# Kernel tuning notes

Measured on AMD Instinct MI355X. Metric: run time of the kernel, lower is better.

Reference implementation:

```python
import jax, jax.numpy as jnp
import numpy as np

B, F, CIN, COUT, K, R = 128, 1024, 16, 16, 4, 2


def setup_inputs() -> dict:
    key = jax.random.key(0)
    k1, k2 = jax.random.split(key)
    ll = jax.random.normal(k1, (B, F, CIN, R), dtype=jnp.float32)
    logits = jax.random.normal(k2, (COUT, CIN, K, K, R), dtype=jnp.float32)
    return {"ll": ll, "logits": logits, "kernel_size": K}


def reference(ll, logits, kernel_size):
    # ll: (B, F, Cin, R); logits: (O, Cin, K, K, R)
    b, f, cin, r = ll.shape
    o = logits.shape[0]
    k = kernel_size
    h = w = int(round(f ** 0.5))
    hb, wb = h // k, w // k
    # normalize weights over input channels (sum_dim=1)
    log_w = jax.nn.log_softmax(logits, axis=1)          # (O, Cin, K, K, R)
    # im2col-like patch reshape: (B, Cin, hb, wb, K, K, R)
    x = jnp.transpose(ll, (0, 2, 1, 3)).reshape(b, cin, hb, k, wb, k, r)
    x = jnp.transpose(x, (0, 1, 2, 4, 3, 5, 6))
    # broadcast-add log weights per kernel position, reduce over Cin
    w_b = log_w[None, :, :, None, None, :, :, :]        # (1, O, Cin, 1, 1, K, K, R)
    out = jax.nn.logsumexp(x[:, None] + w_b, axis=2)    # (B, O, hb, wb, K, K, R)
    # reassemble spatial grid and flatten back to features
    out = jnp.transpose(out, (0, 1, 2, 4, 3, 5, 6)).reshape(b, o, h, w, r)
    out = out.reshape(b, o, f, r)
    return jnp.transpose(out, (0, 2, 1, 3))             # (B, F, O, R)
```

## Files before the change

kernel.cpp:

```cpp
#include <hip/hip_runtime.h>


#define WSTRIDE 520
#define ESTRIDE 36

__global__ __launch_bounds__(256, 4) void sumconv_fused(
    const float* __restrict__ ll, const float* __restrict__ logits,
    float* __restrict__ out) {
  __shared__ float sw[8 * WSTRIDE + 64 * ESTRIDE];
  float* __restrict__ swW = sw;
  float* __restrict__ swE = sw + 8 * WSTRIDE;

  const int tid = threadIdx.x;
  const int blk = blockIdx.x;
  const int f_base = (blk * 64) & 1023;
  const int kkbase = ((f_base >> 5) & 3) * 4;

  {
    const int r = tid & 1, kkloc = (tid >> 1) & 7, o = tid >> 4;
    const int kk = kkbase + kkloc;
    const float* __restrict__ lg = logits + o * 512 + kk * 2 + r;
    float v[16];
    float m = -1e30f;
#pragma unroll
    for (int ci = 0; ci < 16; ++ci) {
      v[ci] = lg[ci * 32];
      m = fmaxf(m, v[ci]);
    }
    float sum = 0.f;
#pragma unroll
    for (int ci = 0; ci < 16; ++ci) {
      v[ci] = __expf(v[ci] - m);
      sum += v[ci];
    }
    const float inv = 1.0f / sum;
#pragma unroll
    for (int ci = 0; ci < 16; ++ci)
      swW[kkloc * WSTRIDE + ci * 32 + o * 2 + r] = v[ci] * inv;
  }

  {
    const float4* __restrict__ src = (const float4*)(ll + (size_t)blk * 2048);
#pragma unroll
    for (int j = 0; j < 2; ++j) {
      const int p = tid + 256 * j;
      const float4 v = src[p];
      const int row = p >> 3, c4 = p & 7;
      *(float4*)(swE + row * ESTRIDE + c4 * 4) =
          make_float4(__expf(v.x), __expf(v.y), __expf(v.z), __expf(v.w));
    }
  }
  __syncthreads();

  const int row = tid >> 2, q = tid & 3;
  const int i = blk * 64 + row;
  const int f = i & 1023;
  const int kk = (((f >> 5) & 3) << 2) | (f & 3);
  const float* __restrict__ wb = swW + (kk & 7) * WSTRIDE + q * 4;
  const float* __restrict__ eb = swE + row * ESTRIDE;

  float Ef[32];
#pragma unroll
  for (int k = 0; k < 8; ++k)
    *(float4*)(Ef + 4 * k) = *(const float4*)(eb + 4 * k);

  float4* __restrict__ op = (float4*)(out + (size_t)i * 32);
#pragma unroll 1
  for (int oo = 0; oo < 2; ++oo) {
    float a00 = 0.f, a01 = 0.f, a10 = 0.f, a11 = 0.f;
#pragma unroll
    for (int ci = 0; ci < 16; ++ci) {
      const float4 w = *(const float4*)(wb + ci * 32 + oo * 16);
      a00 = fmaf(w.x, Ef[2 * ci + 0], a00);
      a01 = fmaf(w.y, Ef[2 * ci + 1], a01);
      a10 = fmaf(w.z, Ef[2 * ci + 0], a10);
      a11 = fmaf(w.w, Ef[2 * ci + 1], a11);
    }
    op[q + 4 * oo] = make_float4(__logf(a00), __logf(a01), __logf(a10), __logf(a11));
  }
}

extern "C" void kernel_launch(void* const* d_in, const int* in_sizes, int n_in,
                              void* d_out, int out_size, void* d_ws, size_t ws_size,
                              hipStream_t stream) {
  const float* ll     = (const float*)d_in[0];
  const float* logits = (const float*)d_in[1];
  float* out = (float*)d_out;
  sumconv_fused<<<2048, 256, 0, stream>>>(ll, logits, out);
}
```

Before: 15.13 us.

## Process four batches per block to amortize weight softmax across batches

Each block now covers 64 features for 4 batch entries instead of 64 features for one, so the per-block log-softmax over logits and the weight reads from shared memory are reused across four batches. The grid shrinks from 2048 to 512 blocks, shared memory for exponentiated inputs grows fourfold, and launch bounds drop to 2 blocks per CU. In exchange, register pressure rises (128 Ef values plus 16 accumulators) and fewer blocks are available to hide latency.

```diff
diff --git a/kernel.cpp b/kernel.cpp
--- a/kernel.cpp
+++ b/kernel.cpp
@@ -4,17 +4,18 @@
 #define WSTRIDE 520
 #define ESTRIDE 36
 
-__global__ __launch_bounds__(256, 4) void sumconv_fused(
+__global__ __launch_bounds__(256, 2) void sumconv_fused(
     const float* __restrict__ ll, const float* __restrict__ logits,
     float* __restrict__ out) {
-  __shared__ float sw[8 * WSTRIDE + 64 * ESTRIDE];
+  __shared__ float sw[8 * WSTRIDE + 256 * ESTRIDE];
   float* __restrict__ swW = sw;
   float* __restrict__ swE = sw + 8 * WSTRIDE;
 
   const int tid = threadIdx.x;
   const int blk = blockIdx.x;
-  const int f_base = (blk * 64) & 1023;
-  const int kkbase = ((f_base >> 5) & 3) * 4;
+  const int f0 = (blk & 15) * 64;
+  const int b0 = (blk >> 4) * 4;
+  const int kkbase = ((f0 >> 5) & 3) * 4;
 
   {
     const int r = tid & 1, kkloc = (tid >> 1) & 7, o = tid >> 4;
@@ -39,44 +40,58 @@
       swW[kkloc * WSTRIDE + ci * 32 + o * 2 + r] = v[ci] * inv;
   }
 
-  {
-    const float4* __restrict__ src = (const float4*)(ll + (size_t)blk * 2048);
 #pragma unroll
-    for (int j = 0; j < 2; ++j) {
-      const int p = tid + 256 * j;
+  for (int j = 0; j < 4; ++j) {
+    const float4* __restrict__ src =
+        (const float4*)(ll + ((size_t)(b0 + j) * 1024 + f0) * 32);
+#pragma unroll
+    for (int m2 = 0; m2 < 2; ++m2) {
+      const int p = tid + 256 * m2;
       const float4 v = src[p];
       const int row = p >> 3, c4 = p & 7;
-      *(float4*)(swE + row * ESTRIDE + c4 * 4) =
+      *(float4*)(swE + (j * 64 + row) * ESTRIDE + c4 * 4) =
           make_float4(__expf(v.x), __expf(v.y), __expf(v.z), __expf(v.w));
     }
   }
   __syncthreads();
 
   const int row = tid >> 2, q = tid & 3;
-  const int i = blk * 64 + row;
-  const int f = i & 1023;
+  const int f = f0 + row;
   const int kk = (((f >> 5) & 3) << 2) | (f & 3);
   const float* __restrict__ wb = swW + (kk & 7) * WSTRIDE + q * 4;
-  const float* __restrict__ eb = swE + row * ESTRIDE;
 
-  float Ef[32];
+  float Ef[4][32];
 #pragma unroll
-  for (int k = 0; k < 8; ++k)
-    *(float4*)(Ef + 4 * k) = *(const float4*)(eb + 4 * k);
+  for (int j = 0; j < 4; ++j) {
+    const float* __restrict__ eb = swE + (j * 64 + row) * ESTRIDE;
+#pragma unroll
+    for (int k = 0; k < 8; ++k)
+      *(float4*)(&Ef[j][4 * k]) = *(const float4*)(eb + 4 * k);
+  }
 
-  float4* __restrict__ op = (float4*)(out + (size_t)i * 32);
-#pragma unroll 1
+#pragma unroll
   for (int oo = 0; oo < 2; ++oo) {
-    float a00 = 0.f, a01 = 0.f, a10 = 0.f, a11 = 0.f;
+    float a[4][4];
+#pragma unroll
+    for (int j = 0; j < 4; ++j)
+      a[j][0] = a[j][1] = a[j][2] = a[j][3] = 0.f;
 #pragma unroll
     for (int ci = 0; ci < 16; ++ci) {
       const float4 w = *(const float4*)(wb + ci * 32 + oo * 16);
-      a00 = fmaf(w.x, Ef[2 * ci + 0], a00);
-      a01 = fmaf(w.y, Ef[2 * ci + 1], a01);
-      a10 = fmaf(w.z, Ef[2 * ci + 0], a10);
-      a11 = fmaf(w.w, Ef[2 * ci + 1], a11);
+#pragma unroll
+      for (int j = 0; j < 4; ++j) {
+        a[j][0] = fmaf(w.x, Ef[j][2 * ci + 0], a[j][0]);
+        a[j][1] = fmaf(w.y, Ef[j][2 * ci + 1], a[j][1]);
+        a[j][2] = fmaf(w.z, Ef[j][2 * ci + 0], a[j][2]);
+        a[j][3] = fmaf(w.w, Ef[j][2 * ci + 1], a[j][3]);
+      }
     }
-    op[q + 4 * oo] = make_float4(__logf(a00), __logf(a01), __logf(a10), __logf(a11));
+#pragma unroll
+    for (int j = 0; j < 4; ++j) {
+      const size_t i = (size_t)(b0 + j) * 1024 + f;
+      ((float4*)(out + i * 32))[q + 4 * oo] = make_float4(
+          __logf(a[j][0]), __logf(a[j][1]), __logf(a[j][2]), __logf(a[j][3]));
+    }
   }
 }
 
@@ -86,5 +101,5 @@
   const float* ll     = (const float*)d_in[0];
   const float* logits = (const float*)d_in[1];
   float* out = (float*)d_out;
-  sumconv_fused<<<2048, 256, 0, stream>>>(ll, logits, out);
+  sumconv_fused<<<512, 256, 0, stream>>>(ll, logits, out);
 }
```

New measurement: 14.07 us. -7.0%, faster.

## Process four batch slabs per block with register-cached weights and prefetched loads

Applied to the files above, without the earlier changes.

Each block now handles four batches of the same 64-feature tile, so the log-softmax weight setup is amortized over four slabs and the weights are held in registers. Input loads for later slabs are issued ahead of time to overlap with compute, using separate LDS slabs and raw barriers in place of __syncthreads. The grid shrinks from 2048 to 512 blocks and launch bounds drop to 2 blocks per SM. In exchange, register pressure and LDS use go up and there is less parallelism to hide latency.

```diff
diff --git a/kernel.cpp b/kernel.cpp
--- a/kernel.cpp
+++ b/kernel.cpp
@@ -3,23 +3,34 @@
 
 #define WSTRIDE 520
 #define ESTRIDE 36
+#define ESLAB (64 * ESTRIDE)
 
-__global__ __launch_bounds__(256, 4) void sumconv_fused(
+#define EXP4(v) make_float4(__expf(v.x), __expf(v.y), __expf(v.z), __expf(v.w))
+
+__global__ __launch_bounds__(256, 2) void sumconv_fused(
     const float* __restrict__ ll, const float* __restrict__ logits,
     float* __restrict__ out) {
-  __shared__ float sw[8 * WSTRIDE + 64 * ESTRIDE];
+  __shared__ float sw[8 * WSTRIDE + 4 * ESLAB];
   float* __restrict__ swW = sw;
   float* __restrict__ swE = sw + 8 * WSTRIDE;
 
   const int tid = threadIdx.x;
   const int blk = blockIdx.x;
-  const int f_base = (blk * 64) & 1023;
-  const int kkbase = ((f_base >> 5) & 3) * 4;
+  const int f0 = (blk & 15) * 64;
+  const int b0 = (blk >> 4) * 4;
+  const int kkbase = ((f0 >> 5) & 3) * 4;
+
+  const float4* __restrict__ s0 = (const float4*)(ll + ((size_t)(b0 + 0) * 1024 + f0) * 32);
+  const float4* __restrict__ s1 = (const float4*)(ll + ((size_t)(b0 + 1) * 1024 + f0) * 32);
+  const float4* __restrict__ s2 = (const float4*)(ll + ((size_t)(b0 + 2) * 1024 + f0) * 32);
+  const float4* __restrict__ s3 = (const float4*)(ll + ((size_t)(b0 + 3) * 1024 + f0) * 32);
+  float4 L0a = s0[tid], L0b = s0[tid + 256];
+  float4 L1a = s1[tid], L1b = s1[tid + 256];
+  float4 L2a, L2b, L3a, L3b;
 
   {
     const int r = tid & 1, kkloc = (tid >> 1) & 7, o = tid >> 4;
-    const int kk = kkbase + kkloc;
-    const float* __restrict__ lg = logits + o * 512 + kk * 2 + r;
+    const float* __restrict__ lg = logits + o * 512 + (kkbase + kkloc) * 2 + r;
     float v[16];
     float m = -1e30f;
 #pragma unroll
@@ -38,46 +49,56 @@
     for (int ci = 0; ci < 16; ++ci)
       swW[kkloc * WSTRIDE + ci * 32 + o * 2 + r] = v[ci] * inv;
   }
-
-  {
-    const float4* __restrict__ src = (const float4*)(ll + (size_t)blk * 2048);
-#pragma unroll
-    for (int j = 0; j < 2; ++j) {
-      const int p = tid + 256 * j;
-      const float4 v = src[p];
-      const int row = p >> 3, c4 = p & 7;
-      *(float4*)(swE + row * ESTRIDE + c4 * 4) =
-          make_float4(__expf(v.x), __expf(v.y), __expf(v.z), __expf(v.w));
-    }
-  }
-  __syncthreads();
+  asm volatile("s_waitcnt lgkmcnt(0)" ::: "memory");
+  __builtin_amdgcn_s_barrier();
 
   const int row = tid >> 2, q = tid & 3;
-  const int i = blk * 64 + row;
-  const int f = i & 1023;
+  const int f = f0 + row;
   const int kk = (((f >> 5) & 3) << 2) | (f & 3);
   const float* __restrict__ wb = swW + (kk & 7) * WSTRIDE + q * 4;
-  const float* __restrict__ eb = swE + row * ESTRIDE;
+  float4 W0[16], W1[16];
+#pragma unroll
+  for (int ci = 0; ci < 16; ++ci) {
+    W0[ci] = *(const float4*)(wb + ci * 32);
+    W1[ci] = *(const float4*)(wb + ci * 32 + 16);
+  }
 
-  float Ef[32];
-#pragma unroll
-  for (int k = 0; k < 8; ++k)
-    *(float4*)(Ef + 4 * k) = *(const float4*)(eb + 4 * k);
+#define SLAB_BODY(J, A, B, ISSUE)                                             \
+  {                                                                           \
+    ISSUE               \
+    float* __restrict__ ew = swE + (J) * ESLAB;                               \
+    *(float4*)(ew + (tid >> 3) * ESTRIDE + (tid & 7) * 4) = EXP4(A);          \
+    *(float4*)(ew + ((tid >> 3) + 32) * ESTRIDE + (tid & 7) * 4) = EXP4(B);   \
+    asm volatile("s_waitcnt lgkmcnt(0)" ::: "memory");                        \
+    __builtin_amdgcn_s_barrier();                                             \
+    const float* __restrict__ ebr = swE + (J) * ESLAB + row * ESTRIDE;        \
+    float Ef[32];                                                             \
+    _Pragma("unroll")                                                         \
+    for (int k2 = 0; k2 < 8; ++k2)                                            \
+      *(float4*)(Ef + 4 * k2) = *(const float4*)(ebr + 4 * k2);               \
+    float4* __restrict__ op =                                                 \
+        (float4*)(out + ((size_t)(b0 + (J)) * 1024 + f) * 32);                \
+    _Pragma("unroll")                                                         \
+    for (int oo = 0; oo < 2; ++oo) {                                          \
+      float a0 = 0.f, a1 = 0.f, a2 = 0.f, a3 = 0.f;                           \
+      _Pragma("unroll")                                                       \
+      for (int ci = 0; ci < 16; ++ci) {                                       \
+        const float4 w = oo ? W1[ci] : W0[ci];                                \
+        a0 = fmaf(w.x, Ef[2 * ci + 0], a0);                                   \
+        a1 = fmaf(w.y, Ef[2 * ci + 1], a1);                                   \
+        a2 = fmaf(w.z, Ef[2 * ci + 0], a2);                                   \
+        a3 = fmaf(w.w, Ef[2 * ci + 1], a3);                                   \
+      }                                                                       \
+      op[q + 4 * oo] =                                                        \
+          make_float4(__logf(a0), __logf(a1), __logf(a2), __logf(a3));        \
+    }                                                                         \
+  }
 
-  float4* __restrict__ op = (float4*)(out + (size_t)i * 32);
-#pragma unroll 1
-  for (int oo = 0; oo < 2; ++oo) {
-    float a00 = 0.f, a01 = 0.f, a10 = 0.f, a11 = 0.f;
-#pragma unroll
-    for (int ci = 0; ci < 16; ++ci) {
-      const float4 w = *(const float4*)(wb + ci * 32 + oo * 16);
-      a00 = fmaf(w.x, Ef[2 * ci + 0], a00);
-      a01 = fmaf(w.y, Ef[2 * ci + 1], a01);
-      a10 = fmaf(w.z, Ef[2 * ci + 0], a10);
-      a11 = fmaf(w.w, Ef[2 * ci + 1], a11);
-    }
-    op[q + 4 * oo] = make_float4(__logf(a00), __logf(a01), __logf(a10), __logf(a11));
-  }
+  SLAB_BODY(0, L0a, L0b, L2a = s2[tid]; L2b = s2[tid + 256];)
+  SLAB_BODY(1, L1a, L1b, L3a = s3[tid]; L3b = s3[tid + 256];)
+  SLAB_BODY(2, L2a, L2b, ;)
+  SLAB_BODY(3, L3a, L3b, ;)
+#undef SLAB_BODY
 }
 
 extern "C" void kernel_launch(void* const* d_in, const int* in_sizes, int n_in,
@@ -86,5 +107,5 @@
   const float* ll     = (const float*)d_in[0];
   const float* logits = (const float*)d_in[1];
   float* out = (float*)d_out;
-  sumconv_fused<<<2048, 256, 0, stream>>>(ll, logits, out);
+  sumconv_fused<<<512, 256, 0, stream>>>(ll, logits, out);
 }
```

Result: faster. 14.16 us (-6.4%).

## Process two batches per block to amortize weight softmax and reuse weights

Applied to the files above, without the earlier changes.

Each block now handles the same 64 features for two batch entries, so the per-block log-softmax of the logits is computed once for twice the work and each shared-memory weight load feeds two batches' FMAs. The ll loads are issued before the softmax to overlap global latency with that computation. The grid is halved, and the full barrier is replaced by an explicit lgkmcnt wait plus s_barrier. The cost is more registers per thread (two 32-float exp arrays and 16 accumulators), which may reduce occupancy, and fewer blocks to fill the device.

```diff
diff --git a/kernel.cpp b/kernel.cpp
--- a/kernel.cpp
+++ b/kernel.cpp
@@ -4,22 +4,28 @@
 #define WSTRIDE 520
 #define ESTRIDE 36
 
+#define EXP4(v) make_float4(__expf(v.x), __expf(v.y), __expf(v.z), __expf(v.w))
+
 __global__ __launch_bounds__(256, 4) void sumconv_fused(
     const float* __restrict__ ll, const float* __restrict__ logits,
     float* __restrict__ out) {
-  __shared__ float sw[8 * WSTRIDE + 64 * ESTRIDE];
-  float* __restrict__ swW = sw;
-  float* __restrict__ swE = sw + 8 * WSTRIDE;
+  __shared__ float swW[8 * WSTRIDE];
+  __shared__ float swE[128 * ESTRIDE];
 
   const int tid = threadIdx.x;
   const int blk = blockIdx.x;
-  const int f_base = (blk * 64) & 1023;
-  const int kkbase = ((f_base >> 5) & 3) * 4;
+  const int f0 = (blk & 15) * 64;
+  const int b0 = (blk >> 4) * 2;
+  const int kkbase = ((f0 >> 5) & 3) * 4;
+
+  const float4* __restrict__ s0 = (const float4*)(ll + ((size_t)(b0 + 0) * 1024 + f0) * 32);
+  const float4* __restrict__ s1 = (const float4*)(ll + ((size_t)(b0 + 1) * 1024 + f0) * 32);
+  const float4 A0 = s0[tid], A1 = s0[tid + 256];
+  const float4 B0 = s1[tid], B1 = s1[tid + 256];
 
   {
     const int r = tid & 1, kkloc = (tid >> 1) & 7, o = tid >> 4;
-    const int kk = kkbase + kkloc;
-    const float* __restrict__ lg = logits + o * 512 + kk * 2 + r;
+    const float* __restrict__ lg = logits + o * 512 + (kkbase + kkloc) * 2 + r;
     float v[16];
     float m = -1e30f;
 #pragma unroll
@@ -40,44 +46,56 @@
   }
 
   {
-    const float4* __restrict__ src = (const float4*)(ll + (size_t)blk * 2048);
+    const int row = tid >> 3, c4 = (tid & 7) * 4;
+    *(float4*)(swE + (row +  0) * ESTRIDE + c4) = EXP4(A0);
+    *(float4*)(swE + (row + 32) * ESTRIDE + c4) = EXP4(A1);
+    *(float4*)(swE + (row + 64) * ESTRIDE + c4) = EXP4(B0);
+    *(float4*)(swE + (row + 96) * ESTRIDE + c4) = EXP4(B1);
+  }
+  asm volatile("s_waitcnt lgkmcnt(0)" ::: "memory");
+  __builtin_amdgcn_s_barrier();
+
+  const int row = tid >> 2, q = tid & 3;
+  const int f = f0 + row;
+  const int kk = (((f >> 5) & 3) << 2) | (f & 3);
+  const float* __restrict__ wb = swW + (kk & 7) * WSTRIDE + q * 4;
+
+  float Ef0[32], Ef1[32];
+  {
+    const float* __restrict__ e0 = swE + row * ESTRIDE;
+    const float* __restrict__ e1 = swE + (64 + row) * ESTRIDE;
 #pragma unroll
-    for (int j = 0; j < 2; ++j) {
-      const int p = tid + 256 * j;
-      const float4 v = src[p];
-      const int row = p >> 3, c4 = p & 7;
-      *(float4*)(swE + row * ESTRIDE + c4 * 4) =
-          make_float4(__expf(v.x), __expf(v.y), __expf(v.z), __expf(v.w));
+    for (int k = 0; k < 8; ++k) {
+      *(float4*)(Ef0 + 4 * k) = *(const float4*)(e0 + 4 * k);
+      *(float4*)(Ef1 + 4 * k) = *(const float4*)(e1 + 4 * k);
     }
   }
-  __syncthreads();
 
-  const int row = tid >> 2, q = tid & 3;
-  const int i = blk * 64 + row;
-  const int f = i & 1023;
-  const int kk = (((f >> 5) & 3) << 2) | (f & 3);
-  const float* __restrict__ wb = swW + (kk & 7) * WSTRIDE + q * 4;
-  const float* __restrict__ eb = swE + row * ESTRIDE;
+  float a[16];
+#pragma unroll
+  for (int t = 0; t < 16; ++t) a[t] = 0.f;
+#pragma unroll
+  for (int ci = 0; ci < 16; ++ci) {
+    const float4 w0 = *(const float4*)(wb + ci * 32);
+    const float4 w1 = *(const float4*)(wb + ci * 32 + 16);
+    const float e00 = Ef0[2 * ci], e01 = Ef0[2 * ci + 1];
+    const float e10 = Ef1[2 * ci], e11 = Ef1[2 * ci + 1];
+    a[0]  = fmaf(w0.x, e00, a[0]);   a[1]  = fmaf(w0.y, e01, a[1]);
+    a[2]  = fmaf(w0.z, e00, a[2]);   a[3]  = fmaf(w0.w, e01, a[3]);
+    a[4]  = fmaf(w0.x, e10, a[4]);   a[5]  = fmaf(w0.y, e11, a[5]);
+    a[6]  = fmaf(w0.z, e10, a[6]);   a[7]  = fmaf(w0.w, e11, a[7]);
+    a[8]  = fmaf(w1.x, e00, a[8]);   a[9]  = fmaf(w1.y, e01, a[9]);
+    a[10] = fmaf(w1.z, e00, a[10]);  a[11] = fmaf(w1.w, e01, a[11]);
+    a[12] = fmaf(w1.x, e10, a[12]);  a[13] = fmaf(w1.y, e11, a[13]);
+    a[14] = fmaf(w1.z, e10, a[14]);  a[15] = fmaf(w1.w, e11, a[15]);
+  }
 
-  float Ef[32];
-#pragma unroll
-  for (int k = 0; k < 8; ++k)
-    *(float4*)(Ef + 4 * k) = *(const float4*)(eb + 4 * k);
-
-  float4* __restrict__ op = (float4*)(out + (size_t)i * 32);
-#pragma unroll 1
-  for (int oo = 0; oo < 2; ++oo) {
-    float a00 = 0.f, a01 = 0.f, a10 = 0.f, a11 = 0.f;
-#pragma unroll
-    for (int ci = 0; ci < 16; ++ci) {
-      const float4 w = *(const float4*)(wb + ci * 32 + oo * 16);
-      a00 = fmaf(w.x, Ef[2 * ci + 0], a00);
-      a01 = fmaf(w.y, Ef[2 * ci + 1], a01);
-      a10 = fmaf(w.z, Ef[2 * ci + 0], a10);
-      a11 = fmaf(w.w, Ef[2 * ci + 1], a11);
-    }
-    op[q + 4 * oo] = make_float4(__logf(a00), __logf(a01), __logf(a10), __logf(a11));
-  }
+  float4* __restrict__ op0 = (float4*)(out + ((size_t)(b0 + 0) * 1024 + f) * 32);
+  float4* __restrict__ op1 = (float4*)(out + ((size_t)(b0 + 1) * 1024 + f) * 32);
+  op0[q]     = make_float4(__logf(a[0]),  __logf(a[1]),  __logf(a[2]),  __logf(a[3]));
+  op1[q]     = make_float4(__logf(a[4]),  __logf(a[5]),  __logf(a[6]),  __logf(a[7]));
+  op0[q + 4] = make_float4(__logf(a[8]),  __logf(a[9]),  __logf(a[10]), __logf(a[11]));
+  op1[q + 4] = make_float4(__logf(a[12]), __logf(a[13]), __logf(a[14]), __logf(a[15]));
 }
 
 extern "C" void kernel_launch(void* const* d_in, const int* in_sizes, int n_in,
@@ -86,5 +104,5 @@
   const float* ll     = (const float*)d_in[0];
   const float* logits = (const float*)d_in[1];
   float* out = (float*)d_out;
-  sumconv_fused<<<2048, 256, 0, stream>>>(ll, logits, out);
+  sumconv_fused<<<1024, 256, 0, stream>>>(ll, logits, out);
 }
```

Result: faster. 13.56 us (median of 2 runs) (-10.4%).
